# Kernel tuning notes

Measured on AMD Instinct MI355X. Metric: run time of the kernel, lower is better.

Reference implementation:

```python
import jax, jax.numpy as jnp
import numpy as np

# Swin block config (matches init_kwargs)
B = 64; H = 28; W = 28; C = 384; NH = 12; WS = 7; SS = 3; HID = 1536
N = WS * WS            # tokens per window (49)
D = C // NH            # head dim (32)
NW = (H // WS) * (W // WS)  # windows per image (16)
SCALE = D ** -0.5


def _rel_pos_index():
    # matches torch.meshgrid default 'ij' indexing
    coords = np.stack(np.meshgrid(np.arange(WS), np.arange(WS), indexing='ij'))
    flat = coords.reshape(2, -1)                      # (2, N)
    rel = flat[:, :, None] - flat[:, None, :]          # (2, N, N)
    rel = rel.transpose(1, 2, 0).copy()                # (N, N, 2)
    rel[:, :, 0] += WS - 1
    rel[:, :, 1] += WS - 1
    rel[:, :, 0] *= 2 * WS - 1
    return rel.sum(-1)                                 # (N, N) int


def _attn_mask():
    img = np.zeros((H, W))
    slices = (slice(0, -WS), slice(-WS, -SS), slice(-SS, None))
    cnt = 0
    for hs in slices:
        for ws in slices:
            img[hs, ws] = cnt
            cnt += 1
    mw = img.reshape(H // WS, WS, W // WS, WS).transpose(0, 2, 1, 3).reshape(-1, N)
    am = mw[:, None, :] - mw[:, :, None]               # (nW, N, N)
    return np.where(am != 0, -100.0, 0.0).astype(np.float32)


def setup_inputs() -> dict:
    key = jax.random.key(0)
    ks = jax.random.split(key, 8)
    p = lambda k, shape: 0.02 * jax.random.normal(k, shape, dtype=jnp.float32)
    return {
        'x_1': jax.random.normal(ks[0], (B, H * W, C), dtype=jnp.float32),
        'act_scaling_factor_1': jnp.ones((1,), jnp.float32),
        'norm1_w': jnp.ones((C,), jnp.float32), 'norm1_b': jnp.zeros((C,), jnp.float32),
        'qkv_w': p(ks[1], (3 * C, C)), 'qkv_b': jnp.zeros((3 * C,), jnp.float32),
        'rel_bias_table': p(ks[2], ((2 * WS - 1) ** 2, NH)),
        'proj_w': p(ks[3], (C, C)), 'proj_b': jnp.zeros((C,), jnp.float32),
        'norm2_w': jnp.ones((C,), jnp.float32), 'norm2_b': jnp.zeros((C,), jnp.float32),
        'fc1_w': p(ks[4], (HID, C)), 'fc1_b': jnp.zeros((HID,), jnp.float32),
        'fc2_w': p(ks[5], (C, HID)), 'fc2_b': jnp.zeros((C,), jnp.float32),
    }


def _ln(x, w, b):
    m = jnp.mean(x, -1, keepdims=True)
    v = jnp.mean((x - m) ** 2, -1, keepdims=True)
    return (x - m) * jax.lax.rsqrt(v + 1e-5) * w + b


def reference(x_1, act_scaling_factor_1, norm1_w, norm1_b, qkv_w, qkv_b,
              rel_bias_table, proj_w, proj_b, norm2_w, norm2_b,
              fc1_w, fc1_b, fc2_w, fc2_b):
    rel_idx = jnp.asarray(_rel_pos_index().reshape(-1))
    mask = jnp.asarray(_attn_mask())
    shortcut = x_1
    h = _ln(x_1, norm1_w, norm1_b).reshape(B, H, W, C)
    h = jnp.roll(h, (-SS, -SS), axis=(1, 2))
    # window partition -> (B*nW, N, C)
    h = h.reshape(B, H // WS, WS, W // WS, WS, C).transpose(0, 1, 3, 2, 4, 5).reshape(-1, N, C)
    qkv = (h @ qkv_w.T + qkv_b).reshape(-1, N, 3, NH, D).transpose(2, 0, 3, 1, 4)
    q, k, v = qkv[0], qkv[1], qkv[2]            # (B_, NH, N, D)
    attn = jnp.einsum('bhnd,bhmd->bhnm', q, k) * SCALE
    bias = rel_bias_table[rel_idx].reshape(N, N, NH).transpose(2, 0, 1)  # (NH, N, N)
    attn = attn + bias[None]
    attn = attn.reshape(B, NW, NH, N, N) + mask[None, :, None]
    attn = jax.nn.softmax(attn.reshape(-1, NH, N, N), axis=-1)
    o = jnp.einsum('bhnm,bhmd->bhnd', attn, v).transpose(0, 2, 1, 3).reshape(-1, N, C)
    o = o @ proj_w.T + proj_b
    # window reverse + unshift
    o = o.reshape(B, H // WS, W // WS, WS, WS, C).transpose(0, 1, 3, 2, 4, 5).reshape(B, H, W, C)
    o = jnp.roll(o, (SS, SS), axis=(1, 2)).reshape(B, H * W, C)
    x2 = shortcut + o
    m = _ln(x2, norm2_w, norm2_b)
    m = jax.nn.gelu(m @ fc1_w.T + fc1_b, approximate=False)
    m = m @ fc2_w.T + fc2_b
    return x2 + m
```

## Files before the change

### kernel.cpp

```cpp
#include <hip/hip_runtime.h>
#include <hip/hip_bf16.h>
#include <math.h>

typedef unsigned short u16;
typedef unsigned int u32;
typedef __attribute__((ext_vector_type(8))) short short8;
typedef __attribute__((ext_vector_type(4))) float f32x4;

__device__ __forceinline__ float b2f(u16 u){ u32 i = ((u32)u)<<16; float f; __builtin_memcpy(&f,&i,4); return f; }
__device__ __forceinline__ u16 f2b(float f){ u32 i; __builtin_memcpy(&i,&f,4); u32 r=(i+0x7FFFu+((i>>16)&1u))>>16; return (u16)r; }
__device__ __forceinline__ int region(int h){ return h<21?0:(h<25?1:2); }

__device__ __forceinline__ int xswz(int bid, int nwg){
  int q = nwg >> 3, r = nwg & 7;
  int xcd = bid & 7, loc = bid >> 3;
  int base = (xcd < r) ? xcd*(q+1) : r*(q+1) + (xcd-r)*q;
  return base + loc;
}

__global__ __launch_bounds__(256) void wcvt_all(
    const float* __restrict__ w0, u16* __restrict__ o0,
    const float* __restrict__ w1, u16* __restrict__ o1,
    const float* __restrict__ w2, u16* __restrict__ o2,
    const float* __restrict__ w3, u16* __restrict__ o3)
{
  int b = blockIdx.x;
  const float* in; u16* out; int ofs;
  if (b < 432){ in=w0; out=o0; ofs=b; }
  else if (b < 576){ in=w1; out=o1; ofs=b-432; }
  else if (b < 1152){ in=w2; out=o2; ofs=b-576; }
  else { in=w3; out=o3; ofs=b-1152; }
  int i = (ofs*256 + threadIdx.x)*4;
  f32x4 v = *(const f32x4*)(in + i);
  u16 o[4];
  #pragma unroll
  for (int e=0;e<4;e++) o[e] = f2b(v[e]);
  *(u32*)(out+i) = (u32)o[0] | ((u32)o[1]<<16);
  *(u32*)(out+i+2) = (u32)o[2] | ((u32)o[3]<<16);
}

__global__ __launch_bounds__(256) void ln1_win(const float* __restrict__ x,
    const float* __restrict__ w, const float* __restrict__ bb, u16* __restrict__ out)
{
  int lane = threadIdx.x & 63;
  int t = blockIdx.x*4 + (threadIdx.x>>6);
  int win = t/49, n = t - win*49;
  int b = win>>4, wi = win&15;
  int r = n/7, c = n - r*7;
  int oh = (wi>>2)*7 + r + 3; if (oh>=28) oh -= 28;
  int ow = (wi&3)*7 + c + 3; if (ow>=28) ow -= 28;
  size_t src = ((size_t)b*784 + oh*28 + ow)*384;
  float v[6];
  #pragma unroll
  for (int p=0;p<3;p++){
    float2 d = *(const float2*)(x + src + 2*lane + 128*p);
    v[2*p] = d.x; v[2*p+1] = d.y;
  }
  float s=0.f, sq=0.f;
  #pragma unroll
  for (int e=0;e<6;e++){ s+=v[e]; sq+=v[e]*v[e]; }
  #pragma unroll
  for (int off=32; off>=1; off>>=1){ s+=__shfl_xor(s,off); sq+=__shfl_xor(sq,off); }
  float mean = s*(1.f/384.f);
  float rstd = rsqrtf(sq*(1.f/384.f)-mean*mean + 1e-5f);
  size_t dst = (size_t)t*384;
  #pragma unroll
  for (int p=0;p<3;p++){
    int col = 2*lane+128*p;
    float2 wd = *(const float2*)(w+col), bd = *(const float2*)(bb+col);
    float y0 = (v[2*p]-mean)*rstd*wd.x + bd.x;
    float y1 = (v[2*p+1]-mean)*rstd*wd.y + bd.y;
    *(u32*)(out + dst + col) = (u32)f2b(y0) | ((u32)f2b(y1)<<16);
  }
}

__global__ __launch_bounds__(256) void ln2_k(const float* __restrict__ x2,
    const float* __restrict__ w, const float* __restrict__ bb, u16* __restrict__ out)
{
  int lane = threadIdx.x & 63;
  int t = blockIdx.x*4 + (threadIdx.x>>6);
  size_t base = (size_t)t*384;
  float v[6];
  #pragma unroll
  for (int p=0;p<3;p++){
    float2 d = *(const float2*)(x2 + base + 2*lane + 128*p);
    v[2*p] = d.x; v[2*p+1] = d.y;
  }
  float s=0.f, sq=0.f;
  #pragma unroll
  for (int e=0;e<6;e++){ s+=v[e]; sq+=v[e]*v[e]; }
  #pragma unroll
  for (int off=32; off>=1; off>>=1){ s+=__shfl_xor(s,off); sq+=__shfl_xor(sq,off); }
  float mean = s*(1.f/384.f);
  float rstd = rsqrtf(sq*(1.f/384.f)-mean*mean + 1e-5f);
  #pragma unroll
  for (int p=0;p<3;p++){
    int col = 2*lane+128*p;
    float2 wd = *(const float2*)(w+col), bd = *(const float2*)(bb+col);
    float y0 = (v[2*p]-mean)*rstd*wd.x + bd.x;
    float y1 = (v[2*p+1]-mean)*rstd*wd.y + bd.y;
    *(u32*)(out + base + col) = (u32)f2b(y0) | ((u32)f2b(y1)<<16);
  }
}

__global__ __launch_bounds__(256) void attn_mfma(const u16* __restrict__ qkv,
    const float* __restrict__ table, u16* __restrict__ out)
{
  __shared__ __align__(16) u16 P[4][4096];
  __shared__ float bsh[4][224];
  int wv = threadIdx.x>>6, lane = threadIdx.x&63;
  int idx = blockIdx.x*4 + wv;
  int winl = idx/12, h = idx - winl*12;
  int wi = winl & 15;
  int g = lane>>4, q15 = lane&15;
  const float SCALE = 0.17677669529663687f;

  for (int e=lane; e<169; e+=64) bsh[wv][e] = table[e*12 + h];

  const u16* base = qkv + (size_t)winl*49*1152 + h*32;

  short8 qa[4], kb[4];
  #pragma unroll
  for (int t=0;t<4;t++){
    int tq = 16*t + q15; if (tq>48) tq = 48;
    qa[t] = *(const short8*)(base + (size_t)tq*1152 + g*8);
    kb[t] = *(const short8*)(base + (size_t)tq*1152 + 384 + g*8);
  }
  f32x4 zero = {0.f,0.f,0.f,0.f};
  f32x4 s[4][4];
  #pragma unroll
  for (int ti=0;ti<4;ti++){
    #pragma unroll
    for (int tj=0;tj<4;tj++) s[ti][tj] = zero;
  }
  #pragma unroll
  for (int ti=0;ti<4;ti++){
    #pragma unroll
    for (int tj=0;tj<4;tj++)
      s[ti][tj] = __builtin_amdgcn_mfma_f32_16x16x32_bf16(qa[ti], kb[tj], s[ti][tj], 0,0,0);
  }

  int hb7 = (wi>>2)*7, wb7 = (wi&3)*7;
  int yj[4], xj[4], ridj[4]; bool kjok[4];
  #pragma unroll
  for (int tj=0;tj<4;tj++){
    int kj = 16*tj + q15;
    kjok[tj] = (kj < 49);
    int y = (kj*37)>>8; int xx = kj - y*7;
    yj[tj] = y; xj[tj] = xx;
    ridj[tj] = region(hb7+y)*3 + region(wb7+xx);
  }
  #pragma unroll
  for (int ti=0;ti<4;ti++){
    #pragma unroll
    for (int r=0;r<4;r++){
      int q = 16*ti + 4*g + r;
      int yi = (q*37)>>8, xi = q - yi*7;
      int ridi = region(hb7+yi)*3 + region(wb7+xi);
      int bb0 = (yi+6)*13 + xi + 6;
      #pragma unroll
      for (int tj=0;tj<4;tj++){
        float v;
        if (kjok[tj]){
          float bias = bsh[wv][bb0 - yj[tj]*13 - xj[tj]];
          v = s[ti][tj][r]*SCALE + bias + ((ridi==ridj[tj]) ? 0.f : -100.f);
        } else v = -1e30f;
        s[ti][tj][r] = v;
      }
    }
  }

  float inv[4][4];
  #pragma unroll
  for (int ti=0;ti<4;ti++){
    #pragma unroll
    for (int r=0;r<4;r++){
      float m = fmaxf(fmaxf(s[ti][0][r], s[ti][1][r]), fmaxf(s[ti][2][r], s[ti][3][r]));
      m = fmaxf(m, __shfl_xor(m,1));
      m = fmaxf(m, __shfl_xor(m,2));
      m = fmaxf(m, __shfl_xor(m,4));
      m = fmaxf(m, __shfl_xor(m,8));
      float sum = 0.f;
      #pragma unroll
      for (int tj=0;tj<4;tj++){
        float e = __expf(s[ti][tj][r] - m);
        s[ti][tj][r] = e; sum += e;
      }
      sum += __shfl_xor(sum,1);
      sum += __shfl_xor(sum,2);
      sum += __shfl_xor(sum,4);
      sum += __shfl_xor(sum,8);
      inv[ti][r] = 1.f/sum;
    }
  }

  u16* Pw = P[wv];
  #pragma unroll
  for (int ti=0;ti<4;ti++){
    #pragma unroll
    for (int r=0;r<4;r++){
      int q = 16*ti + 4*g + r;
      int swz = (q&7)<<4;
      #pragma unroll
      for (int tj=0;tj<4;tj++){
        int kj = 16*tj + q15;
        *(u16*)((char*)Pw + ((q*128 + kj*2) ^ swz)) = f2b(s[ti][tj][r]);
      }
    }
  }
  __syncthreads();

  f32x4 o[4][2];
  #pragma unroll
  for (int ti=0;ti<4;ti++){ o[ti][0]=zero; o[ti][1]=zero; }
  #pragma unroll
  for (int kk=0;kk<2;kk++){
    short8 pa[4];
    #pragma unroll
    for (int ti=0;ti<4;ti++){
      int qq = 16*ti + q15;
      pa[ti] = *(const short8*)((char*)Pw + ((qq*128 + kk*64 + g*16) ^ ((qq&7)<<4)));
    }
    #pragma unroll
    for (int tn=0;tn<2;tn++){
      short8 vb;
      #pragma unroll
      for (int e=0;e<8;e++){
        int tok = kk*32 + g*8 + e; if (tok>48) tok = 48;
        vb[e] = *(const short*)(base + (size_t)tok*1152 + 768 + 16*tn + q15);
      }
      #pragma unroll
      for (int ti=0;ti<4;ti++)
        o[ti][tn] = __builtin_amdgcn_mfma_f32_16x16x32_bf16(pa[ti], vb, o[ti][tn], 0,0,0);
    }
  }

  #pragma unroll
  for (int ti=0;ti<4;ti++){
    #pragma unroll
    for (int r=0;r<4;r++){
      int tok = 16*ti + 4*g + r;
      if (tok < 49){
        float iv = inv[ti][r];
        u16* op = out + ((size_t)(winl*49 + tok))*384 + h*32 + q15;
        op[0]  = f2b(o[ti][0][r]*iv);
        op[16] = f2b(o[ti][1][r]*iv);
      }
    }
  }
}

#define STAGE(b, koff) do { \
  u16* _la = SH + (b)*8192 + wid*512; \
  u16* _lb = SH + (b)*8192 + 4096 + wid*512; \
  __builtin_amdgcn_global_load_lds((const __attribute__((address_space(1))) void*)(gA0+(koff)), \
      (__attribute__((address_space(3))) void*)_la, 16,0,0); \
  __builtin_amdgcn_global_load_lds((const __attribute__((address_space(1))) void*)(gA1+(koff)), \
      (__attribute__((address_space(3))) void*)(_la+2048), 16,0,0); \
  __builtin_amdgcn_global_load_lds((const __attribute__((address_space(1))) void*)(gB0+(koff)), \
      (__attribute__((address_space(3))) void*)_lb, 16,0,0); \
  __builtin_amdgcn_global_load_lds((const __attribute__((address_space(1))) void*)(gB1+(koff)), \
      (__attribute__((address_space(3))) void*)(_lb+2048), 16,0,0); \
} while(0)

#define COMPUTE(b) do { \
  const u16* _Ab = SH + (b)*8192; \
  const u16* _Bb = _Ab + 4096; \
  short8 af[4], bf[4]; \
  _Pragma("unroll") \
  for (int t_=0;t_<4;t_++){ \
    af[t_] = *(const short8*)(_Ab + aidx[t_]); \
    bf[t_] = *(const short8*)(_Bb + bidx[t_]); } \
  __builtin_amdgcn_s_setprio(1); \
  _Pragma("unroll") \
  for (int mi=0;mi<4;mi++){ \
    _Pragma("unroll") \
    for (int ni=0;ni<4;ni++){ \
      acc[mi][ni] = __builtin_amdgcn_mfma_f32_16x16x32_bf16(af[mi], bf[ni], acc[mi][ni], 0,0,0); } } \
  __builtin_amdgcn_s_setprio(0); \
} while(0)

template<int EPI>
__global__ __launch_bounds__(256) void gemm_nt(
    const u16* __restrict__ A, const u16* __restrict__ W,
    const float* __restrict__ bias, u16* __restrict__ outb,
    float* __restrict__ x2, const float* __restrict__ xin,
    float* __restrict__ dout, int rowofs, int N, int K, int ntn)
{
  __shared__ __align__(16) u16 SH[16384];
  int bid = xswz(blockIdx.x, gridDim.x);
  int tm = bid / ntn, tn = bid - tm*ntn;
  int tid = threadIdx.x, lane = tid&63, wid = tid>>6;
  int wm = wid>>1, wn = wid&1;
  int fr = lane&15, fc = lane>>4;

  int s0 = wid*1024 + lane*16;
  int row0 = s0>>6;  int cl0 = ((s0>>4)&3) ^ ((row0>>1)&3);
  int s1b = s0 + 4096;
  int row1 = s1b>>6; int cl1 = ((s1b>>4)&3) ^ ((row1>>1)&3);
  const u16* gA0 = A + (size_t)(tm*128 + row0)*K + cl0*8;
  const u16* gA1 = A + (size_t)(tm*128 + row1)*K + cl1*8;
  const u16* gB0 = W + (size_t)(tn*128 + row0)*K + cl0*8;
  const u16* gB1 = W + (size_t)(tn*128 + row1)*K + cl1*8;

  f32x4 zero = {0.f,0.f,0.f,0.f};
  f32x4 acc[4][4];
  #pragma unroll
  for (int a=0;a<4;a++){
    #pragma unroll
    for (int b=0;b<4;b++) acc[a][b] = zero;
  }
  int aidx[4], bidx[4];
  #pragma unroll
  for (int t_=0;t_<4;t_++){
    int ra = wm*64 + t_*16 + fr;
    aidx[t_] = ra*32 + ((fc ^ ((ra>>1)&3))*8);
    int rb = wn*64 + t_*16 + fr;
    bidx[t_] = rb*32 + ((fc ^ ((rb>>1)&3))*8);
  }

  int NT = K>>5;
  STAGE(0, 0);
  STAGE(1, 32);
  int b = 0;
  for (int t=0; t<NT; ++t){
    if (t < NT-1)  asm volatile("s_waitcnt vmcnt(4)" ::: "memory");
    else           asm volatile("s_waitcnt vmcnt(0)" ::: "memory");
    __builtin_amdgcn_s_barrier();
    __builtin_amdgcn_sched_barrier(0);
    COMPUTE(b);
    __builtin_amdgcn_s_barrier();
    __builtin_amdgcn_sched_barrier(0);
    if (t+2 < NT) STAGE(b, (t+2)*32);
    b ^= 1;
  }

  int colbase = tn*128 + wn*64;
  int rowbase = tm*128 + wm*64;

  if (EPI==0 || EPI==2){
    u16* ep = SH + wid*4096;
    #pragma unroll
    for (int ni=0;ni<4;ni++){
      float bv = bias[colbase + ni*16 + fr];
      #pragma unroll
      for (int mi=0;mi<4;mi++){
        #pragma unroll
        for (int rr=0;rr<4;rr++){
          float v = acc[mi][ni][rr] + bv;
          if (EPI==2) v = 0.5f*v*(1.0f + erff(v*0.70710678118654752f));
          ep[(mi*16 + fc*4 + rr)*64 + ni*16 + fr] = f2b(v);
        }
      }
    }
    int half = lane>>5, c2 = (lane&31)*2;
    #pragma unroll
    for (int it=0; it<32; ++it){
      int lrow = it*2 + half;
      u32 v = *(const u32*)(ep + lrow*64 + c2);
      *(u32*)(outb + (size_t)(rowbase + lrow)*N + colbase + c2) = v;
    }
  } else {
    #pragma unroll
    for (int ni=0;ni<4;ni++){
      int col = colbase + ni*16 + fr;
      float bv = bias[col];
      #pragma unroll
      for (int mi=0;mi<4;mi++){
        #pragma unroll
        for (int rr=0;rr<4;rr++){
          int row = rowbase + mi*16 + fc*4 + rr;
          float v = acc[mi][ni][rr] + bv;
          if (EPI==1){
            int grow = rowofs + row;
            int win = grow/49, n = grow - win*49;
            int bb = win>>4, wi = win&15;
            int hh = (wi>>2)*7 + n/7 + 3; if (hh>=28) hh -= 28;
            int ww = (wi&3)*7 + (n - (n/7)*7) + 3; if (ww>=28) ww -= 28;
            size_t ti = ((size_t)bb*784 + hh*28 + ww)*384 + col;
            x2[ti] = v + xin[ti];
          } else {
            size_t ti = (size_t)row*N + col;
            dout[ti] = v + x2[ti];
          }
        }
      }
    }
  }
}

extern "C" void kernel_launch(void* const* d_in, const int* in_sizes, int n_in,
                              void* d_out, int out_size, void* d_ws, size_t ws_size,
                              hipStream_t stream)
{
  const float* x     = (const float*)d_in[0];
  const float* n1w   = (const float*)d_in[2];
  const float* n1b   = (const float*)d_in[3];
  const float* qkvw  = (const float*)d_in[4];
  const float* qkvb  = (const float*)d_in[5];
  const float* relt  = (const float*)d_in[6];
  const float* projw = (const float*)d_in[7];
  const float* projb = (const float*)d_in[8];
  const float* n2w   = (const float*)d_in[9];
  const float* n2b   = (const float*)d_in[10];
  const float* fc1w  = (const float*)d_in[11];
  const float* fc1b  = (const float*)d_in[12];
  const float* fc2w  = (const float*)d_in[13];
  const float* fc2b  = (const float*)d_in[14];

  int nc;
  if      (ws_size >= 196214784) nc = 1;
  else if (ws_size >= 119144448) nc = 2;
  else                           nc = 4;
  int Mc = 50176/nc;

  char* ws = (char*)d_ws;
  u16* B0    = (u16*)ws;
  u16* qkvc  = (u16*)(ws + 38535168);
  u16* attnc = qkvc + (size_t)Mc*1152;
  u16* fc1c  = qkvc;
  char* wb   = ws + 38535168 + (size_t)Mc*3072;
  u16* wq    = (u16*)(wb);
  u16* wp    = (u16*)(wb + 884736);
  u16* w1    = (u16*)(wb + 1179648);
  u16* w2    = (u16*)(wb + 2359296);
  float* outf = (float*)d_out;

  wcvt_all<<<1728,256,0,stream>>>(qkvw,wq, projw,wp, fc1w,w1, fc2w,w2);

  ln1_win<<<12544,256,0,stream>>>(x, n1w, n1b, B0);

  int mt = Mc/128;
  for (int c=0; c<nc; ++c){
    const u16* a0 = B0 + (size_t)c*Mc*384;
    gemm_nt<0><<<mt*9,256,0,stream>>>(a0, wq, qkvb, qkvc, nullptr, nullptr, nullptr, 0, 1152,384,9);
    attn_mfma<<<Mc/49*12/4,256,0,stream>>>(qkvc, relt, attnc);
    gemm_nt<1><<<mt*3,256,0,stream>>>(attnc, wp, projb, nullptr, outf, x, nullptr, c*Mc, 384,384,3);
  }

  ln2_k<<<12544,256,0,stream>>>(outf, n2w, n2b, B0);

  for (int c=0; c<nc; ++c){
    const u16* a1 = B0 + (size_t)c*Mc*384;
    float* oc = outf + (size_t)c*Mc*384;
    gemm_nt<2><<<mt*12,256,0,stream>>>(a1, w1, fc1b, fc1c, nullptr, nullptr, nullptr, 0, 1536,384,12);
    gemm_nt<3><<<mt*3 ,256,0,stream>>>(fc1c, w2, fc2b, nullptr, oc, nullptr, oc, 0, 384,1536,3);
  }
}
```

Before: 460.6 us.

## Use 256x128 GEMM tiles with 512 threads and triple-buffered LDS pipeline

Moves the GEMM from a 128x128 tile with 256 threads to a 256x128 tile with 8 waves, and from double to triple buffering of the K-slices with adjusted vmcnt waits. Each B tile fetched is now reused across twice as many rows, and the deeper prefetch hides more global latency. In exchange LDS use grows to 72KB per block, which limits how many blocks fit per CU, and the grid is halved, which may leave CUs underfilled. The epilogue staging area is sized by wave id and must still fit 8 waves, and the wm/wn mapping has to cover 4x2 waves correctly. The attention launch grid is also rewritten to an equivalent expression.

```diff
diff --git a/kernel.cpp b/kernel.cpp
--- a/kernel.cpp
+++ b/kernel.cpp
@@ -251,21 +251,18 @@
 }
 
 #define STAGE(b, koff) do { \
-  u16* _la = SH + (b)*8192 + wid*512; \
-  u16* _lb = SH + (b)*8192 + 4096 + wid*512; \
+  u16* _p = SH + (b)*12288; \
   __builtin_amdgcn_global_load_lds((const __attribute__((address_space(1))) void*)(gA0+(koff)), \
-      (__attribute__((address_space(3))) void*)_la, 16,0,0); \
+      (__attribute__((address_space(3))) void*)(_p + tid*8), 16,0,0); \
   __builtin_amdgcn_global_load_lds((const __attribute__((address_space(1))) void*)(gA1+(koff)), \
-      (__attribute__((address_space(3))) void*)(_la+2048), 16,0,0); \
+      (__attribute__((address_space(3))) void*)(_p + 4096 + tid*8), 16,0,0); \
   __builtin_amdgcn_global_load_lds((const __attribute__((address_space(1))) void*)(gB0+(koff)), \
-      (__attribute__((address_space(3))) void*)_lb, 16,0,0); \
-  __builtin_amdgcn_global_load_lds((const __attribute__((address_space(1))) void*)(gB1+(koff)), \
-      (__attribute__((address_space(3))) void*)(_lb+2048), 16,0,0); \
+      (__attribute__((address_space(3))) void*)(_p + 8192 + tid*8), 16,0,0); \
 } while(0)
 
 #define COMPUTE(b) do { \
-  const u16* _Ab = SH + (b)*8192; \
-  const u16* _Bb = _Ab + 4096; \
+  const u16* _Ab = SH + (b)*12288; \
+  const u16* _Bb = _Ab + 8192; \
   short8 af[4], bf[4]; \
   _Pragma("unroll") \
   for (int t_=0;t_<4;t_++){ \
@@ -281,27 +278,25 @@
 } while(0)
 
 template<int EPI>
-__global__ __launch_bounds__(256) void gemm_nt(
+__global__ __launch_bounds__(512) void gemm_nt(
     const u16* __restrict__ A, const u16* __restrict__ W,
     const float* __restrict__ bias, u16* __restrict__ outb,
     float* __restrict__ x2, const float* __restrict__ xin,
     float* __restrict__ dout, int rowofs, int N, int K, int ntn)
 {
-  __shared__ __align__(16) u16 SH[16384];
+  __shared__ __align__(16) u16 SH[36864];
   int bid = xswz(blockIdx.x, gridDim.x);
   int tm = bid / ntn, tn = bid - tm*ntn;
   int tid = threadIdx.x, lane = tid&63, wid = tid>>6;
   int wm = wid>>1, wn = wid&1;
   int fr = lane&15, fc = lane>>4;
 
-  int s0 = wid*1024 + lane*16;
-  int row0 = s0>>6;  int cl0 = ((s0>>4)&3) ^ ((row0>>1)&3);
-  int s1b = s0 + 4096;
-  int row1 = s1b>>6; int cl1 = ((s1b>>4)&3) ^ ((row1>>1)&3);
-  const u16* gA0 = A + (size_t)(tm*128 + row0)*K + cl0*8;
-  const u16* gA1 = A + (size_t)(tm*128 + row1)*K + cl1*8;
-  const u16* gB0 = W + (size_t)(tn*128 + row0)*K + cl0*8;
-  const u16* gB1 = W + (size_t)(tn*128 + row1)*K + cl1*8;
+  int sA0 = tid*16;          int rA0 = sA0>>6; int cA0 = ((sA0>>4)&3) ^ ((rA0>>1)&3);
+  int sA1 = tid*16 + 8192;   int rA1 = sA1>>6; int cA1 = ((sA1>>4)&3) ^ ((rA1>>1)&3);
+  int sB0 = tid*16;          int rB0 = sB0>>6; int cB0 = ((sB0>>4)&3) ^ ((rB0>>1)&3);
+  const u16* gA0 = A + (size_t)(tm*256 + rA0)*K + cA0*8;
+  const u16* gA1 = A + (size_t)(tm*256 + rA1)*K + cA1*8;
+  const u16* gB0 = W + (size_t)(tn*128 + rB0)*K + cB0*8;
 
   f32x4 zero = {0.f,0.f,0.f,0.f};
   f32x4 acc[4][4];
@@ -322,21 +317,23 @@
   int NT = K>>5;
   STAGE(0, 0);
   STAGE(1, 32);
+  STAGE(2, 64);
   int b = 0;
   for (int t=0; t<NT; ++t){
-    if (t < NT-1)  asm volatile("s_waitcnt vmcnt(4)" ::: "memory");
-    else           asm volatile("s_waitcnt vmcnt(0)" ::: "memory");
+    if (t < NT-2)      asm volatile("s_waitcnt vmcnt(6)" ::: "memory");
+    else if (t==NT-2)  asm volatile("s_waitcnt vmcnt(3)" ::: "memory");
+    else               asm volatile("s_waitcnt vmcnt(0)" ::: "memory");
     __builtin_amdgcn_s_barrier();
     __builtin_amdgcn_sched_barrier(0);
     COMPUTE(b);
     __builtin_amdgcn_s_barrier();
     __builtin_amdgcn_sched_barrier(0);
-    if (t+2 < NT) STAGE(b, (t+2)*32);
-    b ^= 1;
+    if (t+3 < NT) STAGE(b, (t+3)*32);
+    if (++b == 3) b = 0;
   }
 
   int colbase = tn*128 + wn*64;
-  int rowbase = tm*128 + wm*64;
+  int rowbase = tm*256 + wm*64;
 
   if (EPI==0 || EPI==2){
     u16* ep = SH + wid*4096;
@@ -430,12 +427,12 @@
 
   ln1_win<<<12544,256,0,stream>>>(x, n1w, n1b, B0);
 
-  int mt = Mc/128;
+  int mt = Mc/256;
   for (int c=0; c<nc; ++c){
     const u16* a0 = B0 + (size_t)c*Mc*384;
-    gemm_nt<0><<<mt*9,256,0,stream>>>(a0, wq, qkvb, qkvc, nullptr, nullptr, nullptr, 0, 1152,384,9);
-    attn_mfma<<<Mc/49*12/4,256,0,stream>>>(qkvc, relt, attnc);
-    gemm_nt<1><<<mt*3,256,0,stream>>>(attnc, wp, projb, nullptr, outf, x, nullptr, c*Mc, 384,384,3);
+    gemm_nt<0><<<mt*9,512,0,stream>>>(a0, wq, qkvb, qkvc, nullptr, nullptr, nullptr, 0, 1152,384,9);
+    attn_mfma<<<Mc/49*3,256,0,stream>>>(qkvc, relt, attnc);
+    gemm_nt<1><<<mt*3,512,0,stream>>>(attnc, wp, projb, nullptr, outf, x, nullptr, c*Mc, 384,384,3);
   }
 
   ln2_k<<<12544,256,0,stream>>>(outf, n2w, n2b, B0);
@@ -443,7 +440,7 @@
   for (int c=0; c<nc; ++c){
     const u16* a1 = B0 + (size_t)c*Mc*384;
     float* oc = outf + (size_t)c*Mc*384;
-    gemm_nt<2><<<mt*12,256,0,stream>>>(a1, w1, fc1b, fc1c, nullptr, nullptr, nullptr, 0, 1536,384,12);
-    gemm_nt<3><<<mt*3 ,256,0,stream>>>(fc1c, w2, fc2b, nullptr, oc, nullptr, oc, 0, 384,1536,3);
-  }
-}
+    gemm_nt<2><<<mt*12,512,0,stream>>>(a1, w1, fc1b, fc1c, nullptr, nullptr, nullptr, 0, 1536,384,12);
+    gemm_nt<3><<<mt*3 ,512,0,stream>>>(fc1c, w2, fc2b, nullptr, oc, nullptr, oc, 0, 384,1536,3);
+  }
+}
```

New measurement: 528.2 us. 1.15x slower.
